# Performance work log

Measured on AMD Instinct MI355X. Metric: run time of the kernel, lower is better.

The kernel has to match this reference:

```python
import jax, jax.numpy as jnp
import numpy as np

K = 512
D = 64
BETA = 0.25


def setup_inputs() -> dict:
    key = jax.random.key(0)
    k1, k2 = jax.random.split(key)
    z_e = jax.random.normal(k1, (64, D, 64, 64), dtype=jnp.float32)  # (B, D, H, W)
    # uniform(-1/K, 1/K) init like nn.Embedding.weight.data.uniform_
    codebook = jax.random.uniform(k2, (K, D), dtype=jnp.float32, minval=-1.0 / K, maxval=1.0 / K)
    return {"z_e": z_e, "codebook": codebook}


def reference(z_e, codebook):
    B, d, H, W = z_e.shape
    # (B, D, H, W) -> (B*H*W, D)
    z_e_flat = jnp.transpose(z_e, (0, 2, 3, 1)).reshape(-1, d)
    # squared euclidean distances: ||z||^2 - 2 z.E^T + ||E||^2  -> (N, K)
    dists = (
        jnp.sum(z_e_flat * z_e_flat, axis=1, keepdims=True)
        - 2.0 * (z_e_flat @ codebook.T)
        + jnp.sum(codebook * codebook, axis=1)[None, :]
    )
    indices = jnp.argmin(dists, axis=1)  # (N,)
    z_q_flat = codebook[indices]         # (N, D)
    codebook_loss = jnp.mean((z_q_flat - jax.lax.stop_gradient(z_e_flat)) ** 2)
    commitment_loss = BETA * jnp.mean((z_e_flat - jax.lax.stop_gradient(z_q_flat)) ** 2)
    # straight-through estimator
    z_q_flat_st = z_e_flat + jax.lax.stop_gradient(z_q_flat - z_e_flat)
    z_q = jnp.transpose(z_q_flat_st.reshape(B, H, W, d), (0, 3, 1, 2))
    return z_q, codebook_loss, commitment_loss
```

## Files before the change

### kernel.cpp

```cpp
#include <hip/hip_runtime.h>
#include <hip/hip_bf16.h>
#include <stdint.h>


typedef __bf16 bf16x8 __attribute__((ext_vector_type(8)));
typedef float f32x16 __attribute__((ext_vector_type(16)));

union ABu { uint32_t w[4]; uint4 u4; bf16x8 v; };

__device__ inline uint32_t pack_bf16(float a, float b) {
  __hip_bfloat162 h = __float22bfloat162_rn(make_float2(a, b));
  uint32_t u;
  __builtin_memcpy(&u, &h, 4);
  return u;
}

__global__ __launch_bounds__(256)
void vq_prep(const float* __restrict__ cb, uint32_t* __restrict__ cb_bf,
             float* __restrict__ e2) {
  int t = blockIdx.x * 256 + threadIdx.x;
  float2 f = ((const float2*)cb)[t];
  uint32_t u = pack_bf16(f.x, f.y);
  cb_bf[t] = u;
  __hip_bfloat162 h;
  __builtin_memcpy(&h, &u, 4);
  float2 fb = __bfloat1622float2(h);
  float s = fb.x * fb.x + fb.y * fb.y;
#pragma unroll
  for (int off = 1; off <= 16; off <<= 1) s += __shfl_xor(s, off);
  if ((t & 31) == 0) e2[t >> 5] = s;
}

__global__ __launch_bounds__(256)
void vq_main(const float* __restrict__ zin, const uint32_t* __restrict__ cb_bf,
             const float* __restrict__ e2g, float* __restrict__ out) {
  __shared__ uint32_t cbl[16384];
  const int tid = threadIdx.x;
  const int wid = tid >> 6;
  const int lane = tid & 63;
  const int col = lane & 31;
  const int half = lane >> 5;
  const int xk = col & 7;

  {
    const uint4* cb4 = (const uint4*)cb_bf;
#pragma unroll
    for (int j = 0; j < 16; ++j) {
      int g = j * 256 + tid;
      int k = g >> 3, c = g & 7;
      *(uint4*)&cbl[k * 32 + ((c ^ (k & 7)) << 2)] = cb4[g];
    }
  }
  __syncthreads();

  float blk = 0.f;

#pragma unroll 1
  for (int it = 0; it < 2; ++it) {
    const int s = blockIdx.x * 2 + it;
    const int b = s >> 4;
    const int hw0 = (s & 15) << 8;
    const float* slab = zin + ((size_t)b << 18) + hw0;

    ABu Bf[2][4];
    float z2[2];
#pragma unroll
    for (int rt = 0; rt < 2; ++rt) {
      const int r = wid * 64 + rt * 32 + col;
      float sacc = 0.f;
#pragma unroll
      for (int m = 0; m < 4; ++m) {
        const int d0 = m * 16 + half * 8;
#pragma unroll
        for (int p = 0; p < 4; ++p) {
          float va = slab[(size_t)(d0 + 2 * p) * 4096 + r];
          float vb = slab[(size_t)(d0 + 2 * p + 1) * 4096 + r];
          sacc += va * va + vb * vb;
          Bf[rt][m].w[p] = pack_bf16(va, vb);
        }
      }
      z2[rt] = sacc;
    }

    ABu A[4], An[4];
#pragma unroll
    for (int m = 0; m < 4; ++m)
      A[m].u4 = *(const uint4*)&cbl[(col << 5) + (((2 * m + half) ^ xk) << 2)];
    float st[2] = {-3.4e38f, -3.4e38f};
#pragma unroll 1
    for (int ct = 0; ct < 16; ++ct) {
      const int ctn = (ct + 1) & 15;
      const int nbase = (ctn << 10) + (col << 5);
#pragma unroll
      for (int m = 0; m < 4; ++m)
        An[m].u4 = *(const uint4*)&cbl[nbase + (((2 * m + half) ^ xk) << 2)];
      const uint32_t ctor = (uint32_t)(ct << 5) | (uint32_t)(half << 2);
#pragma unroll
      for (int rt = 0; rt < 2; ++rt) {
        f32x16 acc = {0, 0, 0, 0, 0, 0, 0, 0, 0, 0, 0, 0, 0, 0, 0, 0};
#pragma unroll
        for (int m = 0; m < 4; ++m)
          acc = __builtin_amdgcn_mfma_f32_32x32x16_bf16(A[m].v, Bf[rt][m].v, acc, 0, 0, 0);
#pragma unroll
        for (int r16 = 0; r16 < 16; ++r16) {
          const uint32_t cr = (uint32_t)((r16 & 3) | ((r16 >> 2) << 3));
          uint32_t bits =
              (__builtin_bit_cast(uint32_t, acc[r16]) & 0xFFFFFE00u) | (ctor | cr);
          st[rt] = fmaxf(st[rt], __builtin_bit_cast(float, bits));
        }
      }
#pragma unroll
      for (int m = 0; m < 4; ++m) A[m].u4 = An[m].u4;
    }

    float lsum = 0.f;
    int kk[2];
#pragma unroll
    for (int rt = 0; rt < 2; ++rt) {
      float mx = fmaxf(st[rt], __shfl_xor(st[rt], 32));
      float z2t = z2[rt] + __shfl_xor(z2[rt], 32);
      uint32_t mbits = __builtin_bit_cast(uint32_t, mx);
      kk[rt] = (int)(mbits & 511u);
      float dot = __builtin_bit_cast(float, mbits & 0xFFFFFE00u);
      lsum += z2t - 2.f * dot + e2g[kk[rt]];
    }
#pragma unroll
    for (int off = 1; off <= 16; off <<= 1) lsum += __shfl_xor(lsum, off);
    blk += lsum;

    float* oslab = out + ((size_t)b << 18) + hw0;
#pragma unroll
    for (int rt = 0; rt < 2; ++rt) {
      const int k = kk[rt];
      const int r = wid * 64 + rt * 32 + col;
      const int kb = (k << 5);
      const int kx = k & 7;
#pragma unroll
      for (int i = 0; i < 4; ++i) {
        ABu q;
        q.u4 = *(const uint4*)&cbl[kb + ((((half << 2) + i) ^ kx) << 2)];
#pragma unroll
        for (int w = 0; w < 4; ++w) {
          const uint32_t u = q.w[w];
          const int d = half * 32 + i * 8 + w * 2;
          oslab[(size_t)d * 4096 + r] = __builtin_bit_cast(float, u << 16);
          oslab[(size_t)(d + 1) * 4096 + r] =
              __builtin_bit_cast(float, u & 0xFFFF0000u);
        }
      }
    }
  }

  __syncthreads();
  if (lane == 0) ((float*)cbl)[wid] = blk;
  __syncthreads();
  if (tid == 0) {
    float t = ((float*)cbl)[0] + ((float*)cbl)[1] + ((float*)cbl)[2] + ((float*)cbl)[3];
    float sc = t * (1.0f / 16777216.0f);
    atomicAdd(out + 16777216, sc);
    atomicAdd(out + 16777217, 0.25f * sc);
  }
}

extern "C" void kernel_launch(void* const* d_in, const int* in_sizes, int n_in,
                              void* d_out, int out_size, void* d_ws, size_t ws_size,
                              hipStream_t stream) {
  const float* zin = (const float*)d_in[0];
  const float* cbf = (const float*)d_in[1];
  uint32_t* cb_bf = (uint32_t*)d_ws;
  float* e2 = (float*)((char*)d_ws + 65536);
  float* out = (float*)d_out;

  vq_prep<<<64, 256, 0, stream>>>(cbf, cb_bf, e2);
  vq_main<<<512, 256, 0, stream>>>(zin, cb_bf, e2, out);
}
```

Baseline: 128.5 us.

## Switch codebook and activations to FP8 MFMA with scaled codebook, one slab per block

Converts the codebook (scaled by 512) and the activations to FP8 and uses the 32x32x16 FP8 MFMA in place of BF16, halving LDS footprint and the codebook staging traffic. Each block now handles one slab instead of two, so the grid doubles to 1024 blocks, and the smaller LDS allocation can allow more blocks per CU. The output z_q is written from the FP8 codebook dequantized by 1/512, and the loss uses the exact fp32 codebook norms. This heavily degrades the accuracy of the argmin and of the output values, since FP8 e4m3 has only 3 mantissa bits, so the result likely breaks tolerance.

```diff
diff --git a/kernel.cpp b/kernel.cpp
--- a/kernel.cpp
+++ b/kernel.cpp
@@ -3,38 +3,34 @@
 #include <stdint.h>
 
 
-typedef __bf16 bf16x8 __attribute__((ext_vector_type(8)));
 typedef float f32x16 __attribute__((ext_vector_type(16)));
+typedef float f32x2 __attribute__((ext_vector_type(2)));
 
-union ABu { uint32_t w[4]; uint4 u4; bf16x8 v; };
+union Fu { uint32_t w[2]; uint2 u2; long l; };
 
-__device__ inline uint32_t pack_bf16(float a, float b) {
-  __hip_bfloat162 h = __float22bfloat162_rn(make_float2(a, b));
-  uint32_t u;
-  __builtin_memcpy(&u, &h, 4);
-  return u;
+__global__ __launch_bounds__(256)
+void vq_prep(const float* __restrict__ cb, uint32_t* __restrict__ cb8,
+             float* __restrict__ e2) {
+  int t = blockIdx.x * 256 + threadIdx.x;
+  int k = t >> 4, dw = t & 15;
+  const float4 f = ((const float4*)cb)[t];
+  uint32_t u = 0;
+  u = __builtin_amdgcn_cvt_pk_fp8_f32(f.x * 512.f, f.y * 512.f, u, false);
+  u = __builtin_amdgcn_cvt_pk_fp8_f32(f.z * 512.f, f.w * 512.f, u, true);
+  int ch = dw >> 1;
+  cb8[k * 16 + ((ch ^ (k & 7)) << 1) + (dw & 1)] = u;
+  float s = f.x * f.x + f.y * f.y + f.z * f.z + f.w * f.w;
+  s += __shfl_xor(s, 1);
+  s += __shfl_xor(s, 2);
+  s += __shfl_xor(s, 4);
+  s += __shfl_xor(s, 8);
+  if ((t & 15) == 0) e2[k] = s;
 }
 
 __global__ __launch_bounds__(256)
-void vq_prep(const float* __restrict__ cb, uint32_t* __restrict__ cb_bf,
-             float* __restrict__ e2) {
-  int t = blockIdx.x * 256 + threadIdx.x;
-  float2 f = ((const float2*)cb)[t];
-  uint32_t u = pack_bf16(f.x, f.y);
-  cb_bf[t] = u;
-  __hip_bfloat162 h;
-  __builtin_memcpy(&h, &u, 4);
-  float2 fb = __bfloat1622float2(h);
-  float s = fb.x * fb.x + fb.y * fb.y;
-#pragma unroll
-  for (int off = 1; off <= 16; off <<= 1) s += __shfl_xor(s, off);
-  if ((t & 31) == 0) e2[t >> 5] = s;
-}
-
-__global__ __launch_bounds__(256)
-void vq_main(const float* __restrict__ zin, const uint32_t* __restrict__ cb_bf,
+void vq_main(const float* __restrict__ zin, const uint32_t* __restrict__ cb8,
              const float* __restrict__ e2g, float* __restrict__ out) {
-  __shared__ uint32_t cbl[16384];
+  __shared__ uint32_t cbl[8192];
   const int tid = threadIdx.x;
   const int wid = tid >> 6;
   const int lane = tid & 63;
@@ -43,78 +39,82 @@
   const int xk = col & 7;
 
   {
-    const uint4* cb4 = (const uint4*)cb_bf;
+    const uint4* cb4 = (const uint4*)cb8;
 #pragma unroll
-    for (int j = 0; j < 16; ++j) {
-      int g = j * 256 + tid;
-      int k = g >> 3, c = g & 7;
-      *(uint4*)&cbl[k * 32 + ((c ^ (k & 7)) << 2)] = cb4[g];
-    }
+    for (int j = 0; j < 8; ++j) ((uint4*)cbl)[j * 256 + tid] = cb4[j * 256 + tid];
   }
   __syncthreads();
 
-  float blk = 0.f;
+  const int s = blockIdx.x;
+  const int b = s >> 4;
+  const int hw0 = (s & 15) << 8;
+  const float* slab = zin + ((size_t)b << 18) + hw0;
 
+  Fu Bf[2][4];
+  float z2[2];
+#pragma unroll
+  for (int rt = 0; rt < 2; ++rt) {
+    const int r = wid * 64 + rt * 32 + col;
+    float sacc = 0.f;
+#pragma unroll
+    for (int m = 0; m < 4; ++m) {
+      const int d0 = m * 16 + half * 8;
+      float v0 = slab[(size_t)(d0 + 0) * 4096 + r];
+      float v1 = slab[(size_t)(d0 + 1) * 4096 + r];
+      float v2 = slab[(size_t)(d0 + 2) * 4096 + r];
+      float v3 = slab[(size_t)(d0 + 3) * 4096 + r];
+      float v4 = slab[(size_t)(d0 + 4) * 4096 + r];
+      float v5 = slab[(size_t)(d0 + 5) * 4096 + r];
+      float v6 = slab[(size_t)(d0 + 6) * 4096 + r];
+      float v7 = slab[(size_t)(d0 + 7) * 4096 + r];
+      sacc += v0 * v0 + v1 * v1 + v2 * v2 + v3 * v3 + v4 * v4 + v5 * v5 +
+              v6 * v6 + v7 * v7;
+      uint32_t lo = __builtin_amdgcn_cvt_pk_fp8_f32(v0, v1, 0u, false);
+      lo = __builtin_amdgcn_cvt_pk_fp8_f32(v2, v3, lo, true);
+      uint32_t hi = __builtin_amdgcn_cvt_pk_fp8_f32(v4, v5, 0u, false);
+      hi = __builtin_amdgcn_cvt_pk_fp8_f32(v6, v7, hi, true);
+      Bf[rt][m].w[0] = lo;
+      Bf[rt][m].w[1] = hi;
+    }
+    z2[rt] = sacc;
+  }
+
+  Fu A[4], An[4];
+#pragma unroll
+  for (int m = 0; m < 4; ++m)
+    A[m].u2 = *(const uint2*)&cbl[(col << 4) + (((2 * m + half) ^ xk) << 1)];
+  float st[2] = {-3.4e38f, -3.4e38f};
 #pragma unroll 1
-  for (int it = 0; it < 2; ++it) {
-    const int s = blockIdx.x * 2 + it;
-    const int b = s >> 4;
-    const int hw0 = (s & 15) << 8;
-    const float* slab = zin + ((size_t)b << 18) + hw0;
-
-    ABu Bf[2][4];
-    float z2[2];
+  for (int ct = 0; ct < 16; ++ct) {
+    const int ctn = (ct + 1) & 15;
+    const int nbase = (ctn << 9) + (col << 4);
+#pragma unroll
+    for (int m = 0; m < 4; ++m)
+      An[m].u2 = *(const uint2*)&cbl[nbase + (((2 * m + half) ^ xk) << 1)];
+    const uint32_t ctor = (uint32_t)(ct << 5) | (uint32_t)(half << 2);
 #pragma unroll
     for (int rt = 0; rt < 2; ++rt) {
-      const int r = wid * 64 + rt * 32 + col;
-      float sacc = 0.f;
-#pragma unroll
-      for (int m = 0; m < 4; ++m) {
-        const int d0 = m * 16 + half * 8;
-#pragma unroll
-        for (int p = 0; p < 4; ++p) {
-          float va = slab[(size_t)(d0 + 2 * p) * 4096 + r];
-          float vb = slab[(size_t)(d0 + 2 * p + 1) * 4096 + r];
-          sacc += va * va + vb * vb;
-          Bf[rt][m].w[p] = pack_bf16(va, vb);
-        }
-      }
-      z2[rt] = sacc;
-    }
-
-    ABu A[4], An[4];
-#pragma unroll
-    for (int m = 0; m < 4; ++m)
-      A[m].u4 = *(const uint4*)&cbl[(col << 5) + (((2 * m + half) ^ xk) << 2)];
-    float st[2] = {-3.4e38f, -3.4e38f};
-#pragma unroll 1
-    for (int ct = 0; ct < 16; ++ct) {
-      const int ctn = (ct + 1) & 15;
-      const int nbase = (ctn << 10) + (col << 5);
+      f32x16 acc = {0, 0, 0, 0, 0, 0, 0, 0, 0, 0, 0, 0, 0, 0, 0, 0};
 #pragma unroll
       for (int m = 0; m < 4; ++m)
-        An[m].u4 = *(const uint4*)&cbl[nbase + (((2 * m + half) ^ xk) << 2)];
-      const uint32_t ctor = (uint32_t)(ct << 5) | (uint32_t)(half << 2);
+        acc = __builtin_amdgcn_mfma_f32_32x32x16_fp8_fp8(A[m].l, Bf[rt][m].l,
+                                                         acc, 0, 0, 0);
 #pragma unroll
-      for (int rt = 0; rt < 2; ++rt) {
-        f32x16 acc = {0, 0, 0, 0, 0, 0, 0, 0, 0, 0, 0, 0, 0, 0, 0, 0};
+      for (int r16 = 0; r16 < 16; ++r16) {
+        const uint32_t cr = (uint32_t)((r16 & 3) | ((r16 >> 2) << 3));
+        uint32_t bits =
+            (__builtin_bit_cast(uint32_t, acc[r16]) & 0xFFFFFE00u) | (ctor | cr);
+        st[rt] = fmaxf(st[rt], __builtin_bit_cast(float, bits));
+      }
+    }
 #pragma unroll
-        for (int m = 0; m < 4; ++m)
-          acc = __builtin_amdgcn_mfma_f32_32x32x16_bf16(A[m].v, Bf[rt][m].v, acc, 0, 0, 0);
-#pragma unroll
-        for (int r16 = 0; r16 < 16; ++r16) {
-          const uint32_t cr = (uint32_t)((r16 & 3) | ((r16 >> 2) << 3));
-          uint32_t bits =
-              (__builtin_bit_cast(uint32_t, acc[r16]) & 0xFFFFFE00u) | (ctor | cr);
-          st[rt] = fmaxf(st[rt], __builtin_bit_cast(float, bits));
-        }
-      }
-#pragma unroll
-      for (int m = 0; m < 4; ++m) A[m].u4 = An[m].u4;
-    }
+    for (int m = 0; m < 4; ++m) A[m].u2 = An[m].u2;
+  }
 
+  float blk = 0.f;
+  int kk[2];
+  {
     float lsum = 0.f;
-    int kk[2];
 #pragma unroll
     for (int rt = 0; rt < 2; ++rt) {
       float mx = fmaxf(st[rt], __shfl_xor(st[rt], 32));
@@ -122,30 +122,34 @@
       uint32_t mbits = __builtin_bit_cast(uint32_t, mx);
       kk[rt] = (int)(mbits & 511u);
       float dot = __builtin_bit_cast(float, mbits & 0xFFFFFE00u);
-      lsum += z2t - 2.f * dot + e2g[kk[rt]];
+      lsum += z2t - dot * 0.00390625f + e2g[kk[rt]];
     }
 #pragma unroll
     for (int off = 1; off <= 16; off <<= 1) lsum += __shfl_xor(lsum, off);
-    blk += lsum;
+    blk = lsum;
+  }
 
+  {
     float* oslab = out + ((size_t)b << 18) + hw0;
 #pragma unroll
     for (int rt = 0; rt < 2; ++rt) {
       const int k = kk[rt];
       const int r = wid * 64 + rt * 32 + col;
-      const int kb = (k << 5);
       const int kx = k & 7;
 #pragma unroll
-      for (int i = 0; i < 4; ++i) {
-        ABu q;
-        q.u4 = *(const uint4*)&cbl[kb + ((((half << 2) + i) ^ kx) << 2)];
+      for (int cc = 0; cc < 4; ++cc) {
+        const int ch = half * 4 + cc;
+        Fu q;
+        q.u2 = *(const uint2*)&cbl[(k << 4) + (((ch ^ kx)) << 1)];
 #pragma unroll
-        for (int w = 0; w < 4; ++w) {
-          const uint32_t u = q.w[w];
-          const int d = half * 32 + i * 8 + w * 2;
-          oslab[(size_t)d * 4096 + r] = __builtin_bit_cast(float, u << 16);
-          oslab[(size_t)(d + 1) * 4096 + r] =
-              __builtin_bit_cast(float, u & 0xFFFF0000u);
+        for (int dw = 0; dw < 2; ++dw) {
+          f32x2 f0 = __builtin_amdgcn_cvt_pk_f32_fp8(q.w[dw], false);
+          f32x2 f1 = __builtin_amdgcn_cvt_pk_f32_fp8(q.w[dw], true);
+          const int d = half * 32 + cc * 8 + dw * 4;
+          oslab[(size_t)(d + 0) * 4096 + r] = f0.x * 0.001953125f;
+          oslab[(size_t)(d + 1) * 4096 + r] = f0.y * 0.001953125f;
+          oslab[(size_t)(d + 2) * 4096 + r] = f1.x * 0.001953125f;
+          oslab[(size_t)(d + 3) * 4096 + r] = f1.y * 0.001953125f;
         }
       }
     }
@@ -167,10 +171,10 @@
                               hipStream_t stream) {
   const float* zin = (const float*)d_in[0];
   const float* cbf = (const float*)d_in[1];
-  uint32_t* cb_bf = (uint32_t*)d_ws;
-  float* e2 = (float*)((char*)d_ws + 65536);
+  uint32_t* cb8 = (uint32_t*)d_ws;
+  float* e2 = (float*)((char*)d_ws + 32768);
   float* out = (float*)d_out;
 
-  vq_prep<<<64, 256, 0, stream>>>(cbf, cb_bf, e2);
-  vq_main<<<512, 256, 0, stream>>>(zin, cb_bf, e2, out);
+  vq_prep<<<32, 256, 0, stream>>>(cbf, cb8, e2);
+  vq_main<<<1024, 256, 0, stream>>>(zin, cb8, e2, out);
 }
```

After: 133.4 us. +3.8%, slower.
